# Performance work log

Hardware: AMD Instinct MI355X
Metric: run time of the kernel (lower is better)

Reference implementation:

```python
import jax, jax.numpy as jnp
import numpy as np

BINS = 64
MIN_VAL, MAX_VAL = 0.0, 1.0


def soft_histogram(x, bins=BINS, min_val=MIN_VAL, max_val=MAX_VAL):
    # x: (B, C, H, W)
    B, C, H, W = x.shape
    x_flat = x.reshape(B, C, -1)                       # (B, C, HW)
    bin_width = (max_val - min_val) / bins
    centers = jnp.linspace(min_val + bin_width / 2, max_val - bin_width / 2, bins,
                           dtype=x.dtype)              # (bins,)
    sigma = bin_width
    # broadcasted Gaussian kernel weights, reduced over pixels -> (B, C, bins)
    diff = x_flat[..., None] - centers                 # (B, C, HW, bins)
    weights = jnp.exp(-(diff ** 2) / (2.0 * sigma ** 2))
    hist = weights.sum(axis=2)                         # (B, C, bins)
    hist = hist / (hist.sum(axis=-1, keepdims=True) + 1e-8)
    return hist


def setup_inputs() -> dict:
    key = jax.random.key(0)
    k1, k2 = jax.random.split(key)
    pred = jax.random.uniform(k1, (4, 3, 256, 256), dtype=jnp.float32)
    target = jax.random.uniform(k2, (4, 3, 256, 256), dtype=jnp.float32)
    return {"pred": pred, "target": target}


def reference(pred, target):
    pred_hist = soft_histogram(pred, BINS)
    target_hist = soft_histogram(target, BINS)
    pred_cdf = jnp.cumsum(pred_hist, axis=-1)
    target_cdf = jnp.cumsum(target_hist, axis=-1)
    return jnp.mean(jnp.abs(pred_cdf - target_cdf))
```

## Files before the change

kernel.cpp:

```cpp
#include <hip/hip_runtime.h>
#include <hip/hip_bf16.h>


#define BINS 64
#define NCH 12
#define HW 65536
#define BPC 32
#define PIX_PER_BLOCK (HW / BPC)
#define THREADS 256
#define PIX_PER_THREAD (PIX_PER_BLOCK / THREADS)

__device__ __forceinline__ float fast_exp2(float x) {
#if __has_builtin(__builtin_amdgcn_exp2f)
    return __builtin_amdgcn_exp2f(x);
#else
    return exp2f(x);
#endif
}

__global__ void zero_ws(float* ws, int n) {
    int i = blockIdx.x * blockDim.x + threadIdx.x;
    if (i < n) ws[i] = 0.0f;
}

__global__ __launch_bounds__(THREADS) void hist_kernel(
        const float* __restrict__ pred,
        const float* __restrict__ target,
        float* __restrict__ hist) {
    const int blk   = blockIdx.x;
    const int ch    = blk / BPC;
    const int chunk = blk % BPC;
    const float* src = (ch < NCH) ? (pred + (size_t)ch * HW)
                                  : (target + (size_t)(ch - NCH) * HW);
    const int base = chunk * PIX_PER_BLOCK + threadIdx.x;

    const float S  = 0.84932180028801904f;
    const float XS = 64.0f * S;

    float acc[BINS];
    #pragma unroll
    for (int j = 0; j < BINS; ++j) acc[j] = 0.0f;

    for (int p = 0; p < PIX_PER_THREAD; ++p) {
        float x  = src[base + p * THREADS];
        float xs = x * XS;
        #pragma unroll
        for (int j = 0; j < BINS; ++j) {
            float u = xs - (j + 0.5f) * S;
            acc[j] += fast_exp2(-(u * u));
        }
    }

    const int lane = threadIdx.x & 63;
    #pragma unroll
    for (int k = 32; k >= 1; k >>= 1) {
        const bool hi = (lane & k) != 0;
        #pragma unroll
        for (int i = 0; i < k; ++i) {
            float keepv = hi ? acc[i + k] : acc[i];
            float sendv = hi ? acc[i] : acc[i + k];
            acc[i] = keepv + __shfl_xor(sendv, k, 64);
        }
    }
    float wave_sum = acc[0];

    __shared__ float bh[BINS];
    if (threadIdx.x < BINS) bh[threadIdx.x] = 0.0f;
    __syncthreads();
    atomicAdd(&bh[lane], wave_sum);
    __syncthreads();
    if (threadIdx.x < BINS)
        atomicAdd(&hist[ch * BINS + threadIdx.x], bh[threadIdx.x]);
}

__global__ __launch_bounds__(NCH * 64) void final_kernel(
        const float* __restrict__ hist, float* __restrict__ out) {
    const int w    = threadIdx.x >> 6;
    const int lane = threadIdx.x & 63;

    float ph = hist[w * BINS + lane];
    float th = hist[(NCH + w) * BINS + lane];

    float ps = ph, ts = th;
    #pragma unroll
    for (int d = 1; d < 64; d <<= 1) {
        float a = __shfl_up(ps, d, 64);
        float b = __shfl_up(ts, d, 64);
        if (lane >= d) { ps += a; ts += b; }
    }
    float ptot = __shfl(ps, 63, 64);
    float ttot = __shfl(ts, 63, 64);
    float pc = ps / (ptot + 1e-8f);
    float tc = ts / (ttot + 1e-8f);
    float dv = fabsf(pc - tc);

    #pragma unroll
    for (int k = 32; k >= 1; k >>= 1) dv += __shfl_xor(dv, k, 64);

    __shared__ float warr[NCH];
    if (lane == 0) warr[w] = dv;
    __syncthreads();
    if (threadIdx.x == 0) {
        float s = 0.0f;
        #pragma unroll
        for (int i = 0; i < NCH; ++i) s += warr[i];
        out[0] = s / (float)(NCH * BINS);
    }
}

extern "C" void kernel_launch(void* const* d_in, const int* in_sizes, int n_in,
                              void* d_out, int out_size, void* d_ws, size_t ws_size,
                              hipStream_t stream) {
    const float* pred   = (const float*)d_in[0];
    const float* target = (const float*)d_in[1];
    float* hist = (float*)d_ws;
    float* out  = (float*)d_out;

    zero_ws<<<dim3((2 * NCH * BINS + 255) / 256), dim3(256), 0, stream>>>(
        hist, 2 * NCH * BINS);
    hist_kernel<<<dim3(2 * NCH * BPC), dim3(THREADS), 0, stream>>>(
        pred, target, hist);
    final_kernel<<<dim3(1), dim3(NCH * 64), 0, stream>>>(hist, out);
}
```

Before: 77.79 us.

## Factor Gaussian exps via geometric recurrence and fuse finalize into last block

Rewrites the per-bin Gaussian so each group of 8 adjacent bins needs only two exp2 calls. The other seven weights come from powers of a shared ratio times precomputed constants, exploiting exp(-(u-k)^2/2) = exp(-u^2/2)·exp(uk)·exp(-k^2/2). The separate zero and final kernels are removed: a memset clears the workspace, and the last block to finish (found through an atomic counter) computes the CDF loss. This cuts transcendental throughput pressure and launch overhead, at the cost of some precision loss for far-from-center bins and extra multiplies.

```diff
diff --git a/kernel.cpp b/kernel.cpp
--- a/kernel.cpp
+++ b/kernel.cpp
@@ -6,6 +6,7 @@
 #define NCH 12
 #define HW 65536
 #define BPC 32
+#define NBLK (2 * NCH * BPC)
 #define PIX_PER_BLOCK (HW / BPC)
 #define THREADS 256
 #define PIX_PER_THREAD (PIX_PER_BLOCK / THREADS)
@@ -18,15 +19,48 @@
 #endif
 }
 
-__global__ void zero_ws(float* ws, int n) {
-    int i = blockIdx.x * blockDim.x + threadIdx.x;
-    if (i < n) ws[i] = 0.0f;
+#define K2 0.36787944117144233f
+#define K3 0.049787068367863944f
+#define K4 0.0024787521766663585f
+#define K5 4.5399929762484854e-05f
+#define K6 3.059023205018258e-07f
+#define K7 7.582560427911907e-10f
+#define LOG2E 1.4426950408889634f
+#define LOG2E_H 0.7213475204444817f
+
+__device__ __forceinline__ void eval_pixel(float t, float* acc) {
+    #pragma unroll
+    for (int s = 0; s < 8; ++s) {
+        const float c = (float)(8 * s) + 0.5f;
+        float u  = t - c;
+        float um = fminf(u, 13.0f);
+        float w0 = fast_exp2(-(u * u) * LOG2E_H);
+        float m  = fast_exp2(fmaf(um, LOG2E, -0.5f * LOG2E));
+        float m2 = m * m;
+        float m3 = m2 * m;
+        float m4 = m2 * m2;
+        float m5 = m3 * m2;
+        float m6 = m3 * m3;
+        float m7 = m4 * m3;
+        float p2 = w0 * K2, p3 = w0 * K3, p4 = w0 * K4;
+        float p5 = w0 * K5, p6 = w0 * K6, p7 = w0 * K7;
+        acc[8 * s + 0] += w0;
+        acc[8 * s + 1] = fmaf(w0, m,  acc[8 * s + 1]);
+        acc[8 * s + 2] = fmaf(p2, m2, acc[8 * s + 2]);
+        acc[8 * s + 3] = fmaf(p3, m3, acc[8 * s + 3]);
+        acc[8 * s + 4] = fmaf(p4, m4, acc[8 * s + 4]);
+        acc[8 * s + 5] = fmaf(p5, m5, acc[8 * s + 5]);
+        acc[8 * s + 6] = fmaf(p6, m6, acc[8 * s + 6]);
+        acc[8 * s + 7] = fmaf(p7, m7, acc[8 * s + 7]);
+    }
 }
 
-__global__ __launch_bounds__(THREADS) void hist_kernel(
+__global__ __launch_bounds__(THREADS) void fused_kernel(
         const float* __restrict__ pred,
         const float* __restrict__ target,
-        float* __restrict__ hist) {
+        float* __restrict__ hist,
+        unsigned int* __restrict__ counter,
+        float* __restrict__ out) {
     const int blk   = blockIdx.x;
     const int ch    = blk / BPC;
     const int chunk = blk % BPC;
@@ -34,21 +68,14 @@
                                   : (target + (size_t)(ch - NCH) * HW);
     const int base = chunk * PIX_PER_BLOCK + threadIdx.x;
 
-    const float S  = 0.84932180028801904f;
-    const float XS = 64.0f * S;
-
     float acc[BINS];
     #pragma unroll
     for (int j = 0; j < BINS; ++j) acc[j] = 0.0f;
 
+    #pragma unroll 2
     for (int p = 0; p < PIX_PER_THREAD; ++p) {
-        float x  = src[base + p * THREADS];
-        float xs = x * XS;
-        #pragma unroll
-        for (int j = 0; j < BINS; ++j) {
-            float u = xs - (j + 0.5f) * S;
-            acc[j] += fast_exp2(-(u * u));
-        }
+        float t = src[base + p * THREADS] * 64.0f;
+        eval_pixel(t, acc);
     }
 
     const int lane = threadIdx.x & 63;
@@ -65,47 +92,46 @@
     float wave_sum = acc[0];
 
     __shared__ float bh[BINS];
+    __shared__ int is_last;
     if (threadIdx.x < BINS) bh[threadIdx.x] = 0.0f;
     __syncthreads();
     atomicAdd(&bh[lane], wave_sum);
     __syncthreads();
     if (threadIdx.x < BINS)
         atomicAdd(&hist[ch * BINS + threadIdx.x], bh[threadIdx.x]);
-}
 
-__global__ __launch_bounds__(NCH * 64) void final_kernel(
-        const float* __restrict__ hist, float* __restrict__ out) {
-    const int w    = threadIdx.x >> 6;
-    const int lane = threadIdx.x & 63;
+    __threadfence();
+    if (threadIdx.x == 0) {
+        unsigned prev = __hip_atomic_fetch_add(counter, 1u, __ATOMIC_ACQ_REL,
+                                               __HIP_MEMORY_SCOPE_AGENT);
+        is_last = (prev == NBLK - 1);
+    }
+    __syncthreads();
+    if (!is_last) return;
 
-    float ph = hist[w * BINS + lane];
-    float th = hist[(NCH + w) * BINS + lane];
-
-    float ps = ph, ts = th;
-    #pragma unroll
-    for (int d = 1; d < 64; d <<= 1) {
-        float a = __shfl_up(ps, d, 64);
-        float b = __shfl_up(ts, d, 64);
-        if (lane >= d) { ps += a; ts += b; }
+    const int w = threadIdx.x >> 6;
+    float local = 0.0f;
+    for (int pch = w; pch < NCH; pch += 4) {
+        float ps = hist[pch * BINS + lane];
+        float ts = hist[(NCH + pch) * BINS + lane];
+        #pragma unroll
+        for (int d = 1; d < 64; d <<= 1) {
+            float a = __shfl_up(ps, d, 64);
+            float b = __shfl_up(ts, d, 64);
+            if (lane >= d) { ps += a; ts += b; }
+        }
+        float ptot = __shfl(ps, 63, 64);
+        float ttot = __shfl(ts, 63, 64);
+        float dv = fabsf(ps / (ptot + 1e-8f) - ts / (ttot + 1e-8f));
+        #pragma unroll
+        for (int k = 32; k >= 1; k >>= 1) dv += __shfl_xor(dv, k, 64);
+        local += dv;
     }
-    float ptot = __shfl(ps, 63, 64);
-    float ttot = __shfl(ts, 63, 64);
-    float pc = ps / (ptot + 1e-8f);
-    float tc = ts / (ttot + 1e-8f);
-    float dv = fabsf(pc - tc);
-
-    #pragma unroll
-    for (int k = 32; k >= 1; k >>= 1) dv += __shfl_xor(dv, k, 64);
-
-    __shared__ float warr[NCH];
-    if (lane == 0) warr[w] = dv;
+    __shared__ float wsum[4];
+    if (lane == 0) wsum[w] = local;
     __syncthreads();
-    if (threadIdx.x == 0) {
-        float s = 0.0f;
-        #pragma unroll
-        for (int i = 0; i < NCH; ++i) s += warr[i];
-        out[0] = s / (float)(NCH * BINS);
-    }
+    if (threadIdx.x == 0)
+        out[0] = (wsum[0] + wsum[1] + wsum[2] + wsum[3]) * (1.0f / (NCH * BINS));
 }
 
 extern "C" void kernel_launch(void* const* d_in, const int* in_sizes, int n_in,
@@ -114,11 +140,10 @@
     const float* pred   = (const float*)d_in[0];
     const float* target = (const float*)d_in[1];
     float* hist = (float*)d_ws;
-    float* out  = (float*)d_out;
+    unsigned int* counter = (unsigned int*)((char*)d_ws + NCH * 2 * BINS * 4);
+    float* out = (float*)d_out;
 
-    zero_ws<<<dim3((2 * NCH * BINS + 255) / 256), dim3(256), 0, stream>>>(
-        hist, 2 * NCH * BINS);
-    hist_kernel<<<dim3(2 * NCH * BPC), dim3(THREADS), 0, stream>>>(
-        pred, target, hist);
-    final_kernel<<<dim3(1), dim3(NCH * 64), 0, stream>>>(hist, out);
+    hipMemsetAsync(d_ws, 0, NCH * 2 * BINS * 4 + 4, stream);
+    fused_kernel<<<dim3(NBLK), dim3(THREADS), 0, stream>>>(
+        pred, target, hist, counter, out);
 }
```

New measurement: 126.3 us. +62.3%, slower.
